# Performance work log

Hardware: AMD Instinct MI355X
Metric: run time of the kernel (lower is better)

The kernel has to match this reference:

```python
import jax, jax.numpy as jnp
import numpy as np

B, S, H = 2, 2048, 1024
E, K, F = 64, 8, 512
NORM_TOPK = True
CAP_FACTOR = 2.0


def setup_inputs() -> dict:
    key = jax.random.key(0)
    k0, k1, k2, k3, k4 = jax.random.split(key, 5)
    s_h = 1.0 / np.sqrt(H)
    s_f = 1.0 / np.sqrt(F)
    return {
        "hidden_states": jax.random.normal(k0, (B, S, H), jnp.float32),
        "w_gate": jax.random.normal(k1, (H, E), jnp.float32) * s_h,  # gate: Linear(H->E), no bias
        "w1": jax.random.normal(k2, (E, H, F), jnp.float32) * s_h,   # gate_proj per expert
        "w3": jax.random.normal(k3, (E, H, F), jnp.float32) * s_h,   # up_proj per expert
        "w2": jax.random.normal(k4, (E, F, H), jnp.float32) * s_f,   # down_proj per expert
    }


def reference(hidden_states, w_gate, w1, w3, w2):
    b, s, h = hidden_states.shape
    e = w_gate.shape[1]
    t = b * s
    x = hidden_states.reshape(t, h)
    router_logits = x @ w_gate                                   # [T, E]
    probs = jax.nn.softmax(router_logits.astype(jnp.float32), axis=-1)
    topw, sel = jax.lax.top_k(probs, K)                          # [T, K]
    if NORM_TOPK:
        topw = topw / jnp.sum(topw, axis=-1, keepdims=True)
    topw = topw.astype(x.dtype)

    a = t * K                                                    # total assignments
    c = int(CAP_FACTOR * a / e)                                  # static per-expert capacity
    sel_flat = sel.reshape(a)
    w_flat = topw.reshape(a)
    tok = jnp.repeat(jnp.arange(t), K)
    order = jnp.argsort(sel_flat, stable=True)                   # group assignments by expert
    e_s, t_s, w_s = sel_flat[order], tok[order], w_flat[order]
    counts = jnp.bincount(sel_flat, length=e)
    starts = jnp.cumsum(counts) - counts
    pos = jnp.arange(a) - starts[e_s]                            # position within expert group
    valid = pos < c
    slot = jnp.where(valid, e_s * c + pos, e * c)                # overflow -> dropped sentinel slot

    # dispatch: gather tokens into per-expert contiguous buffer [E, C, H]
    buf = jnp.zeros((e * c + 1, h), x.dtype).at[slot].set(x[t_s])
    xb = buf[: e * c].reshape(e, c, h)
    # grouped gated-SiLU MLP per expert
    g = jnp.einsum('ech,ehf->ecf', xb, w1)
    u = jnp.einsum('ech,ehf->ecf', xb, w3)
    yb = jnp.einsum('ecf,efh->ech', jax.nn.silu(g) * u, w2).reshape(e * c, h)
    # combine: weighted scatter-add back to tokens
    contrib = yb[jnp.minimum(slot, e * c - 1)] * (w_s * valid.astype(x.dtype))[:, None]
    out = jnp.zeros((t, h), x.dtype).at[t_s].add(contrib)
    return out.reshape(b, s, h), router_logits
```

## Files before the change

kernel.cpp:

```cpp
#include <hip/hip_runtime.h>
#include <hip/hip_bf16.h>

#define T_TOK 4096
#define H_DIM 1024
#define E_EXP 64
#define TOPK  8
#define F_DIM 512
#define CAP   1024
#define A_TOT (T_TOK * TOPK)

typedef _Float16 f16;
typedef _Float16 f16x8 __attribute__((ext_vector_type(8)));
typedef float    f32x4 __attribute__((ext_vector_type(4)));

__global__ __launch_bounds__(256) void pack_all_kernel(
    const float* __restrict__ w1, const float* __restrict__ w3,
    const float* __restrict__ w2,
    f16* __restrict__ w1p, f16* __restrict__ w3p, f16* __restrict__ w2p)
{
    const int tid  = threadIdx.x;
    const int lane = tid & 63, wvi = tid >> 6;
    int pid = blockIdx.x * 4 + wvi;
    const float* src; f16* dst; int Nd, kb, kbs, nps;
    if (pid < 32768)      { src = w1; dst = w1p; Nd = 512;  kb = 32; kbs = 5; nps = 4; }
    else if (pid < 65536) { src = w3; dst = w3p; Nd = 512;  kb = 32; kbs = 5; nps = 4; pid -= 32768; }
    else                  { src = w2; dst = w2p; Nd = 1024; kb = 16; kbs = 4; nps = 5; pid -= 65536; }
    const int kt  = pid & (kb - 1);
    const int en  = pid >> kbs;
    const int ntp = en & ((1 << nps) - 1);
    const int e   = en >> nps;
    const int Kd  = kb << 5;
    const int jj = lane & 15, qq = lane >> 4;
    const float* s = src + ((size_t)e * Kd + kt * 32 + qq * 8) * Nd + ntp * 32 + jj;
    f16x8 v0, v1;
    #pragma unroll
    for (int j = 0; j < 8; ++j) {
        float a = s[(size_t)j * Nd];
        float b = s[(size_t)j * Nd + 16];
        v0[j] = (f16)a;
        v1[j] = (f16)b;
    }
    size_t c0 = (size_t)(e * (Nd >> 4) + ntp * 2) * kb + kt;
    *(f16x8*)(dst + c0 * 512 + lane * 8)        = v0;
    *(f16x8*)(dst + (c0 + kb) * 512 + lane * 8) = v1;
}

__global__ __launch_bounds__(256) void router_kernel(
    const float* __restrict__ x, const float* __restrict__ wg,
    float* __restrict__ logits_out, int* __restrict__ sel,
    float* __restrict__ wgtA, f16* __restrict__ xh)
{
    __shared__ float xs[16][128];
    __shared__ float ls[16][65];
    const int tid = threadIdx.x;
    const int e  = tid & 63;
    const int tg = tid >> 6;
    const int tb = blockIdx.x * 16;

    float acc[4] = {0.f, 0.f, 0.f, 0.f};
    for (int h0 = 0; h0 < H_DIM; h0 += 128) {
        {
            int r  = tid >> 4;
            int c0 = (tid & 15) * 8;
            const float4* src = (const float4*)(x + (size_t)(tb + r) * H_DIM + h0 + c0);
            float4 v0 = src[0], v1 = src[1];
            *(float4*)&xs[r][c0]     = v0;
            *(float4*)&xs[r][c0 + 4] = v1;
            f16x8 hv;
            hv[0] = (f16)v0.x; hv[1] = (f16)v0.y; hv[2] = (f16)v0.z; hv[3] = (f16)v0.w;
            hv[4] = (f16)v1.x; hv[5] = (f16)v1.y; hv[6] = (f16)v1.z; hv[7] = (f16)v1.w;
            *(f16x8*)(xh + (size_t)(tb + r) * H_DIM + h0 + c0) = hv;
        }
        __syncthreads();
        for (int hh = 0; hh < 128; ++hh) {
            float w = wg[(size_t)(h0 + hh) * E_EXP + e];
            #pragma unroll
            for (int i = 0; i < 4; ++i)
                acc[i] = fmaf(xs[tg * 4 + i][hh], w, acc[i]);
        }
        __syncthreads();
    }
    #pragma unroll
    for (int i = 0; i < 4; ++i) {
        int tt = tg * 4 + i;
        logits_out[(size_t)(tb + tt) * E_EXP + e] = acc[i];
        ls[tt][e] = acc[i];
    }
    __syncthreads();
    if (tid < 16) {
        int tt = tid;
        float lv[8]; int li[8];
        for (int k = 0; k < 8; ++k) {
            float m = -1e30f; int mi = 0;
            for (int j = 0; j < 64; ++j) {
                float v = ls[tt][j];
                if (v > m) { m = v; mi = j; }
            }
            lv[k] = m; li[k] = mi;
            ls[tt][mi] = -1e30f;
        }
        float s = 0.f, wv[8];
        for (int k = 0; k < 8; ++k) { wv[k] = __expf(lv[k] - lv[0]); s += wv[k]; }
        float inv = 1.f / s;
        for (int k = 0; k < 8; ++k) {
            int a = (tb + tt) * TOPK + k;
            sel[a]  = li[k];
            wgtA[a] = wv[k] * inv;
        }
    }
}

__global__ __launch_bounds__(256) void build_lists_kernel(
    const int* __restrict__ sel,
    int* __restrict__ tok_list, int* __restrict__ slotA,
    int* __restrict__ counts)
{
    __shared__ int sc[256];
    const int e = blockIdx.x;
    const int tid = threadIdx.x;
    const int per = A_TOT / 256;
    const int a0 = tid * per;
    int cnt = 0;
    for (int i = 0; i < per; ++i) cnt += (sel[a0 + i] == e) ? 1 : 0;
    sc[tid] = cnt;
    __syncthreads();
    for (int s = 1; s < 256; s <<= 1) {
        int v = (tid >= s) ? sc[tid - s] : 0;
        __syncthreads();
        sc[tid] += v;
        __syncthreads();
    }
    int total = sc[255];
    int pos = sc[tid] - cnt;
    if (tid == 0) counts[e] = (total < CAP) ? total : CAP;
    for (int i = 0; i < per; ++i) {
        int a = a0 + i;
        if (sel[a] == e) {
            if (pos < CAP) {
                tok_list[e * CAP + pos] = a >> 3;
                slotA[a] = e * CAP + pos;
            } else {
                slotA[a] = -1;
            }
            pos++;
        }
    }
}

#define MFMA16(a, b, c) __builtin_amdgcn_mfma_f32_16x16x32_f16(a, b, c, 0, 0, 0)

__global__ __launch_bounds__(256) void gemm1_kernel(
    const f16* __restrict__ xh, const f16* __restrict__ w1p,
    const f16* __restrict__ w3p, const int* __restrict__ tok_list,
    const int* __restrict__ counts, f16* __restrict__ P)
{
    const int id = blockIdx.x;
    const int x7 = id & 7, r = id >> 3;
    const int ft = r & 7, mt = (r >> 3) & 15, eh = r >> 7;
    const int e = x7 + 8 * eh;
    const int cnt = counts[e];
    const int m0 = mt * 64;
    if (m0 >= cnt) return;
    const int bf = ft * 64;

    __shared__ f16 Xs[2][64][64];
    __shared__ int tok_s[64];

    const int tid = threadIdx.x;
    const int lane = tid & 63, wv = tid >> 6;
    const int jj = lane & 15, qq = lane >> 4;
    const int sr = tid >> 3, sc = (tid & 7) * 8;
    const int swz_w = ((tid & 7) ^ (sr & 7)) * 8;
    const int x8 = jj & 7;
    const int s0 = (qq ^ x8) * 8;
    const int s1 = ((qq + 4) ^ x8) * 8;

    if (tid < 64) {
        int m = m0 + tid;
        tok_s[tid] = (m < cnt) ? tok_list[e * CAP + m] : tok_list[e * CAP];
    }
    __syncthreads();
    const size_t rowA = (size_t)tok_s[sr] * H_DIM + sc;
    const size_t rowB = (size_t)tok_s[sr + 32] * H_DIM + sc;

    const int nt = ft * 4 + wv;
    const f16* w1a = w1p + ((size_t)(e * 32 + nt) * 32) * 512 + lane * 8;
    const f16* w3a = w3p + ((size_t)(e * 32 + nt) * 32) * 512 + lane * 8;

    f32x4 accG[4], accU[4];
    #pragma unroll
    for (int i = 0; i < 4; ++i) {
        accG[i] = (f32x4){0.f, 0.f, 0.f, 0.f};
        accU[i] = (f32x4){0.f, 0.f, 0.f, 0.f};
    }

    {
        f16x8 a = *(const f16x8*)(xh + rowA);
        f16x8 b = *(const f16x8*)(xh + rowB);
        *(f16x8*)&Xs[0][sr][swz_w]      = a;
        *(f16x8*)&Xs[0][sr + 32][swz_w] = b;
    }
    f16x8 cG0 = *(const f16x8*)(w1a);
    f16x8 cG1 = *(const f16x8*)(w1a + 512);
    f16x8 cU0 = *(const f16x8*)(w3a);
    f16x8 cU1 = *(const f16x8*)(w3a + 512);

    #pragma unroll
    for (int it = 0; it < 16; ++it) {
        const int k0 = it * 64;
        __syncthreads();
        f16x8 xn0, xn1, nG0, nG1, nU0, nU1;
        if (it < 15) {
            xn0 = *(const f16x8*)(xh + rowA + k0 + 64);
            xn1 = *(const f16x8*)(xh + rowB + k0 + 64);
            size_t kg = (size_t)(2 * it + 2) * 512;
            nG0 = *(const f16x8*)(w1a + kg);
            nG1 = *(const f16x8*)(w1a + kg + 512);
            nU0 = *(const f16x8*)(w3a + kg);
            nU1 = *(const f16x8*)(w3a + kg + 512);
        }
        const int buf = it & 1;
        #pragma unroll
        for (int m2 = 0; m2 < 4; ++m2) {
            f16x8 a0 = *(const f16x8*)&Xs[buf][m2 * 16 + jj][s0];
            f16x8 a1 = *(const f16x8*)&Xs[buf][m2 * 16 + jj][s1];
            accG[m2] = MFMA16(a0, cG0, accG[m2]);
            accU[m2] = MFMA16(a0, cU0, accU[m2]);
            accG[m2] = MFMA16(a1, cG1, accG[m2]);
            accU[m2] = MFMA16(a1, cU1, accU[m2]);
        }
        if (it < 15) {
            *(f16x8*)&Xs[buf ^ 1][sr][swz_w]      = xn0;
            *(f16x8*)&Xs[buf ^ 1][sr + 32][swz_w] = xn1;
            cG0 = nG0; cG1 = nG1; cU0 = nU0; cU1 = nU1;
        }
    }
    #pragma unroll
    for (int m2 = 0; m2 < 4; ++m2) {
        #pragma unroll
        for (int rr = 0; rr < 4; ++rr) {
            int row = m2 * 16 + qq * 4 + rr;
            float gg = accG[m2][rr], u = accU[m2][rr];
            float p = gg / (1.f + __expf(-gg)) * u;
            P[(size_t)(e * CAP + m0 + row) * F_DIM + bf + wv * 16 + jj] = (f16)p;
        }
    }
}

__global__ __launch_bounds__(256) void gemm2_kernel(
    const f16* __restrict__ P, const f16* __restrict__ w2p,
    const int* __restrict__ counts, f16* __restrict__ Y)
{
    const int id = blockIdx.x;
    const int x7 = id & 7, r = id >> 3;
    const int ht = r & 7, mt = (r >> 3) & 15, eh = r >> 7;
    const int e = x7 + 8 * eh;
    const int cnt = counts[e];
    const int m0 = mt * 64;
    if (m0 >= cnt) return;
    const int h0 = ht * 128;

    __shared__ f16 Ps[2][64][64];

    const int tid = threadIdx.x;
    const int lane = tid & 63, wv = tid >> 6;
    const int jj = lane & 15, qq = lane >> 4;
    const int sr = tid >> 3, sc = (tid & 7) * 8;
    const int swz_w = ((tid & 7) ^ (sr & 7)) * 8;
    const int x8 = jj & 7;
    const int s0 = (qq ^ x8) * 8;
    const int s1 = ((qq + 4) ^ x8) * 8;

    const size_t pbase = (size_t)(e * CAP + m0) * F_DIM;
    const f16* wA = w2p + ((size_t)(e * 64 + ht * 8 + wv) * 16) * 512 + lane * 8;
    const f16* wB = w2p + ((size_t)(e * 64 + ht * 8 + wv + 4) * 16) * 512 + lane * 8;

    f32x4 accA[4], accB[4];
    #pragma unroll
    for (int i = 0; i < 4; ++i) {
        accA[i] = (f32x4){0.f, 0.f, 0.f, 0.f};
        accB[i] = (f32x4){0.f, 0.f, 0.f, 0.f};
    }

    {
        f16x8 a = *(const f16x8*)(P + pbase + (size_t)sr * F_DIM + sc);
        f16x8 b = *(const f16x8*)(P + pbase + (size_t)(sr + 32) * F_DIM + sc);
        *(f16x8*)&Ps[0][sr][swz_w]      = a;
        *(f16x8*)&Ps[0][sr + 32][swz_w] = b;
    }
    f16x8 cA0 = *(const f16x8*)(wA);
    f16x8 cA1 = *(const f16x8*)(wA + 512);
    f16x8 cB0 = *(const f16x8*)(wB);
    f16x8 cB1 = *(const f16x8*)(wB + 512);

    #pragma unroll
    for (int it = 0; it < 8; ++it) {
        const int k0 = it * 64;
        __syncthreads();
        f16x8 pn0, pn1, nA0, nA1, nB0, nB1;
        if (it < 7) {
            pn0 = *(const f16x8*)(P + pbase + (size_t)sr * F_DIM + k0 + 64 + sc);
            pn1 = *(const f16x8*)(P + pbase + (size_t)(sr + 32) * F_DIM + k0 + 64 + sc);
            size_t kg = (size_t)(2 * it + 2) * 512;
            nA0 = *(const f16x8*)(wA + kg);
            nA1 = *(const f16x8*)(wA + kg + 512);
            nB0 = *(const f16x8*)(wB + kg);
            nB1 = *(const f16x8*)(wB + kg + 512);
        }
        const int buf = it & 1;
        #pragma unroll
        for (int m2 = 0; m2 < 4; ++m2) {
            f16x8 a0 = *(const f16x8*)&Ps[buf][m2 * 16 + jj][s0];
            f16x8 a1 = *(const f16x8*)&Ps[buf][m2 * 16 + jj][s1];
            accA[m2] = MFMA16(a0, cA0, accA[m2]);
            accB[m2] = MFMA16(a0, cB0, accB[m2]);
            accA[m2] = MFMA16(a1, cA1, accA[m2]);
            accB[m2] = MFMA16(a1, cB1, accB[m2]);
        }
        if (it < 7) {
            *(f16x8*)&Ps[buf ^ 1][sr][swz_w]      = pn0;
            *(f16x8*)&Ps[buf ^ 1][sr + 32][swz_w] = pn1;
            cA0 = nA0; cA1 = nA1; cB0 = nB0; cB1 = nB1;
        }
    }
    f16* yb = Y + (size_t)(e * CAP + m0) * H_DIM + h0 + wv * 16 + jj;
    #pragma unroll
    for (int m2 = 0; m2 < 4; ++m2) {
        #pragma unroll
        for (int rr = 0; rr < 4; ++rr) {
            int row = m2 * 16 + qq * 4 + rr;
            yb[(size_t)row * H_DIM]      = (f16)accA[m2][rr];
            yb[(size_t)row * H_DIM + 64] = (f16)accB[m2][rr];
        }
    }
}

__global__ __launch_bounds__(256) void combine_kernel(
    const f16* __restrict__ Y, const int* __restrict__ slotA,
    const float* __restrict__ wgtA, float* __restrict__ out)
{
    const int tid = threadIdx.x;
    const int t  = blockIdx.x * 2 + (tid >> 7);
    const int hc = (tid & 127) * 8;
    float acc[8] = {0.f, 0.f, 0.f, 0.f, 0.f, 0.f, 0.f, 0.f};
    const int base = t * TOPK;
    #pragma unroll
    for (int k = 0; k < 8; ++k) {
        int s   = slotA[base + k];
        float w = wgtA[base + k];
        if (s >= 0) {
            f16x8 y = *(const f16x8*)(Y + (size_t)s * H_DIM + hc);
            #pragma unroll
            for (int j = 0; j < 8; ++j) acc[j] += w * (float)y[j];
        }
    }
    float4 o0 = {acc[0], acc[1], acc[2], acc[3]};
    float4 o1 = {acc[4], acc[5], acc[6], acc[7]};
    *(float4*)(out + (size_t)t * H_DIM + hc)     = o0;
    *(float4*)(out + (size_t)t * H_DIM + hc + 4) = o1;
}

extern "C" void kernel_launch(void* const* d_in, const int* in_sizes, int n_in,
                              void* d_out, int out_size, void* d_ws, size_t ws_size,
                              hipStream_t stream) {
    const float* x  = (const float*)d_in[0];
    const float* wg = (const float*)d_in[1];
    const float* w1 = (const float*)d_in[2];
    const float* w3 = (const float*)d_in[3];
    const float* w2 = (const float*)d_in[4];

    float* out    = (float*)d_out;
    float* logits = out + (size_t)T_TOK * H_DIM;

    char* ws = (char*)d_ws;
    int*   sel      = (int*)  (ws);
    float* wgtA     = (float*)(ws + (128 << 10));
    int*   tok_list = (int*)  (ws + (256 << 10));
    int*   slotA    = (int*)  (ws + (512 << 10));
    int*   counts   = (int*)  (ws + (768 << 10));
    f16*   xh       = (f16*)  (ws + (size_t)(1 << 20));
    f16*   P        = (f16*)  (ws + (size_t)(9 << 20));
    f16*   w1p      = (f16*)  (ws + (size_t)(73 << 20));
    f16*   w3p      = (f16*)  (ws + (size_t)(137 << 20));
    f16*   w2p      = (f16*)  (ws + (size_t)(201 << 20));
    f16*   Y        = (f16*)  (ws + (size_t)(73 << 20));

    pack_all_kernel<<<24576, 256, 0, stream>>>(w1, w3, w2, w1p, w3p, w2p);
    router_kernel<<<T_TOK / 16, 256, 0, stream>>>(x, wg, logits, sel, wgtA, xh);
    build_lists_kernel<<<E_EXP, 256, 0, stream>>>(sel, tok_list, slotA, counts);
    gemm1_kernel<<<8192, 256, 0, stream>>>(xh, w1p, w3p, tok_list, counts, P);
    gemm2_kernel<<<8192, 256, 0, stream>>>(P, w2p, counts, Y);
    combine_kernel<<<T_TOK / 2, 256, 0, stream>>>(Y, slotA, wgtA, out);
}
```

Before: 655.4 us.

## Split weight packing into per-tensor launches and restructure router to 4 tokens per block

The single fused weight-pack kernel becomes three launches of a parameterized pack kernel, which removes per-wave branching on the source tensor. The router now handles 4 tokens per block instead of 16. Each wave loads a full token row into shared memory once and computes one token's 64 logits over all of H with two accumulators, replacing the chunked loop and its repeated barriers. This gives 4x more router blocks for better occupancy, but each block rereads the full gate weight matrix, so total gate-weight traffic goes up.

```diff
diff --git a/kernel.cpp b/kernel.cpp
--- a/kernel.cpp
+++ b/kernel.cpp
@@ -10,21 +10,17 @@
 #define A_TOT (T_TOK * TOPK)
 
 typedef _Float16 f16;
+typedef _Float16 f16x4 __attribute__((ext_vector_type(4)));
 typedef _Float16 f16x8 __attribute__((ext_vector_type(8)));
 typedef float    f32x4 __attribute__((ext_vector_type(4)));
 
-__global__ __launch_bounds__(256) void pack_all_kernel(
-    const float* __restrict__ w1, const float* __restrict__ w3,
-    const float* __restrict__ w2,
-    f16* __restrict__ w1p, f16* __restrict__ w3p, f16* __restrict__ w2p)
+__global__ __launch_bounds__(256) void pack_w_kernel(
+    const float* __restrict__ src, f16* __restrict__ dst,
+    int Nd, int kb, int kbs, int nps)
 {
     const int tid  = threadIdx.x;
     const int lane = tid & 63, wvi = tid >> 6;
-    int pid = blockIdx.x * 4 + wvi;
-    const float* src; f16* dst; int Nd, kb, kbs, nps;
-    if (pid < 32768)      { src = w1; dst = w1p; Nd = 512;  kb = 32; kbs = 5; nps = 4; }
-    else if (pid < 65536) { src = w3; dst = w3p; Nd = 512;  kb = 32; kbs = 5; nps = 4; pid -= 32768; }
-    else                  { src = w2; dst = w2p; Nd = 1024; kb = 16; kbs = 4; nps = 5; pid -= 65536; }
+    const int pid = blockIdx.x * 4 + wvi;
     const int kt  = pid & (kb - 1);
     const int en  = pid >> kbs;
     const int ntp = en & ((1 << nps) - 1);
@@ -50,60 +46,53 @@
     float* __restrict__ logits_out, int* __restrict__ sel,
     float* __restrict__ wgtA, f16* __restrict__ xh)
 {
-    __shared__ float xs[16][128];
-    __shared__ float ls[16][65];
-    const int tid = threadIdx.x;
+    __shared__ float xs[4][1024];
+    __shared__ float ls[4][65];
+    const int tid = threadIdx.x;
+    const int tt = tid >> 6;
     const int e  = tid & 63;
-    const int tg = tid >> 6;
-    const int tb = blockIdx.x * 16;
-
-    float acc[4] = {0.f, 0.f, 0.f, 0.f};
-    for (int h0 = 0; h0 < H_DIM; h0 += 128) {
-        {
-            int r  = tid >> 4;
-            int c0 = (tid & 15) * 8;
-            const float4* src = (const float4*)(x + (size_t)(tb + r) * H_DIM + h0 + c0);
-            float4 v0 = src[0], v1 = src[1];
-            *(float4*)&xs[r][c0]     = v0;
-            *(float4*)&xs[r][c0 + 4] = v1;
-            f16x8 hv;
-            hv[0] = (f16)v0.x; hv[1] = (f16)v0.y; hv[2] = (f16)v0.z; hv[3] = (f16)v0.w;
-            hv[4] = (f16)v1.x; hv[5] = (f16)v1.y; hv[6] = (f16)v1.z; hv[7] = (f16)v1.w;
-            *(f16x8*)(xh + (size_t)(tb + r) * H_DIM + h0 + c0) = hv;
-        }
-        __syncthreads();
-        for (int hh = 0; hh < 128; ++hh) {
-            float w = wg[(size_t)(h0 + hh) * E_EXP + e];
-            #pragma unroll
-            for (int i = 0; i < 4; ++i)
-                acc[i] = fmaf(xs[tg * 4 + i][hh], w, acc[i]);
-        }
-        __syncthreads();
-    }
+    const int tb = blockIdx.x * 4;
+
     #pragma unroll
     for (int i = 0; i < 4; ++i) {
-        int tt = tg * 4 + i;
-        logits_out[(size_t)(tb + tt) * E_EXP + e] = acc[i];
-        ls[tt][e] = acc[i];
+        int idx = i * 256 + tid;
+        int r = idx >> 8, c4 = (idx & 255) * 4;
+        float4 v = *(const float4*)(x + (size_t)(tb + r) * H_DIM + c4);
+        *(float4*)&xs[r][c4] = v;
+        f16x4 hv;
+        hv[0] = (f16)v.x; hv[1] = (f16)v.y; hv[2] = (f16)v.z; hv[3] = (f16)v.w;
+        *(f16x4*)(xh + (size_t)(tb + r) * H_DIM + c4) = hv;
     }
     __syncthreads();
-    if (tid < 16) {
-        int tt = tid;
+
+    float a0 = 0.f, a1 = 0.f;
+    #pragma unroll 8
+    for (int h = 0; h < H_DIM; h += 2) {
+        a0 = fmaf(xs[tt][h],     wg[(size_t)h * E_EXP + e],       a0);
+        a1 = fmaf(xs[tt][h + 1], wg[(size_t)(h + 1) * E_EXP + e], a1);
+    }
+    float acc = a0 + a1;
+    logits_out[(size_t)(tb + tt) * E_EXP + e] = acc;
+    ls[tt][e] = acc;
+    __syncthreads();
+
+    if (tid < 4) {
+        int t4 = tid;
         float lv[8]; int li[8];
         for (int k = 0; k < 8; ++k) {
             float m = -1e30f; int mi = 0;
             for (int j = 0; j < 64; ++j) {
-                float v = ls[tt][j];
+                float v = ls[t4][j];
                 if (v > m) { m = v; mi = j; }
             }
             lv[k] = m; li[k] = mi;
-            ls[tt][mi] = -1e30f;
+            ls[t4][mi] = -1e30f;
         }
         float s = 0.f, wv[8];
         for (int k = 0; k < 8; ++k) { wv[k] = __expf(lv[k] - lv[0]); s += wv[k]; }
         float inv = 1.f / s;
         for (int k = 0; k < 8; ++k) {
-            int a = (tb + tt) * TOPK + k;
+            int a = (tb + t4) * TOPK + k;
             sel[a]  = li[k];
             wgtA[a] = wv[k] * inv;
         }
@@ -385,8 +374,10 @@
     f16*   w2p      = (f16*)  (ws + (size_t)(201 << 20));
     f16*   Y        = (f16*)  (ws + (size_t)(73 << 20));
 
-    pack_all_kernel<<<24576, 256, 0, stream>>>(w1, w3, w2, w1p, w3p, w2p);
-    router_kernel<<<T_TOK / 16, 256, 0, stream>>>(x, wg, logits, sel, wgtA, xh);
+    pack_w_kernel<<<8192, 256, 0, stream>>>(w1, w1p, 512,  32, 5, 4);
+    pack_w_kernel<<<8192, 256, 0, stream>>>(w3, w3p, 512,  32, 5, 4);
+    pack_w_kernel<<<8192, 256, 0, stream>>>(w2, w2p, 1024, 16, 4, 5);
+    router_kernel<<<T_TOK / 4, 256, 0, stream>>>(x, wg, logits, sel, wgtA, xh);
     build_lists_kernel<<<E_EXP, 256, 0, stream>>>(sel, tok_list, slotA, counts);
     gemm1_kernel<<<8192, 256, 0, stream>>>(xh, w1p, w3p, tok_list, counts, P);
     gemm2_kernel<<<8192, 256, 0, stream>>>(P, w2p, counts, Y);
```

Result: faster. 640.6 us (-2.3%).
